# Performance work log

Measured on AMD Instinct MI355X. Metric: run time of the kernel, lower is better.

## Reference

```python
import jax, jax.numpy as jnp
import numpy as np

NUM_HEADS = 16
WINDOW = 128
PERSIST = 16


def setup_inputs() -> dict:
    key = jax.random.key(0)
    ks = jax.random.split(key, 6)
    B, S, D, L = 2, 2048, 2048, 512
    sd = 1.0 / np.sqrt(D)
    sl = 1.0 / np.sqrt(L)
    return {
        "x": jax.random.normal(ks[0], (B, S, D), dtype=jnp.float32),
        "Wq": jax.random.normal(ks[1], (D, D), dtype=jnp.float32) * sd,
        "Wkv": jax.random.normal(ks[2], (D, L), dtype=jnp.float32) * sd,
        "Wk": jax.random.normal(ks[3], (L, D), dtype=jnp.float32) * sl,
        "Wv": jax.random.normal(ks[4], (L, D), dtype=jnp.float32) * sl,
        "Wo": jax.random.normal(ks[5], (D, D), dtype=jnp.float32) * sd,
    }


def reference(x, Wq, Wkv, Wk, Wv, Wo):
    B, S, D = x.shape
    H = NUM_HEADS
    hd = D // H
    scale = hd ** -0.5

    q = (x @ Wq).reshape(B, S, H, hd)
    kv_latent = x @ Wkv                      # MLA-style latent bottleneck
    k = (kv_latent @ Wk).reshape(B, S, H, hd)
    v = (kv_latent @ Wv).reshape(B, S, H, hd)

    # causal + sliding-window + persistent attention-sink mask
    qi = jnp.arange(S)[:, None]
    ki = jnp.arange(S)[None, :]
    mask = (ki <= qi) & ((qi - ki < WINDOW) | (ki < PERSIST))  # [S,S]

    scores = jnp.einsum("bqhd,bkhd->bhqk", q, k) * scale
    scores = jnp.where(mask[None, None], scores, jnp.finfo(scores.dtype).min)
    attn = jax.nn.softmax(scores, axis=-1)
    out = jnp.einsum("bhqk,bkhd->bqhd", attn, v).reshape(B, S, D)
    return out @ Wo
```

## Files before the change

### kernel.cpp

```cpp
#include <hip/hip_runtime.h>

typedef float f32x4 __attribute__((ext_vector_type(4)));
typedef float f32x16 __attribute__((ext_vector_type(16)));
typedef __bf16 bf16x8 __attribute__((ext_vector_type(8)));

__device__ __forceinline__ short f2bf(float f) {
    union { float f; unsigned u; } x; x.f = f;
    unsigned r = x.u + 0x7fffu + ((x.u >> 16) & 1u);
    return (short)(r >> 16);
}

__device__ __forceinline__ void store_out(float* p, float v) { *p = v; }
__device__ __forceinline__ void store_out(short* p, float v) { *p = f2bf(v); }

__device__ __forceinline__ void gload_lds16(const short* g, short* l) {
    __builtin_amdgcn_global_load_lds(
        (__attribute__((address_space(1))) void*)(void*)g,
        (__attribute__((address_space(3))) void*)l, 16, 0, 0);
}

__global__ void prep_all(const float* __restrict__ x, short* __restrict__ xb,
                         const float* __restrict__ Wq, const float* __restrict__ Wkv,
                         short* __restrict__ WqkvT) {
    __shared__ float tile[32][33];
    int id = blockIdx.x;
    const int t = threadIdx.x;
    if (id < 8192) {
        const int i = id * 256 + t;
        float4 v = ((const float4*)x)[i];
        ((short4*)xb)[i] = make_short4(f2bf(v.x), f2bf(v.y), f2bf(v.z), f2bf(v.w));
        return;
    }
    id -= 8192;
    const float* in; short* out; int R, C, xt, yt;
    if (id < 4096) { in = Wq;  out = WqkvT; R = 2048; C = 2048; xt = id & 63; yt = id >> 6; }
    else           { id -= 4096; in = Wkv; out = WqkvT + (size_t)2048 * 2048;
                     R = 2048; C = 512; xt = id & 15; yt = id >> 4; }
    const int c0 = xt * 32, r0 = yt * 32;
    const int tx = t & 31, ty = t >> 5;
#pragma unroll
    for (int i = 0; i < 32; i += 8)
        tile[ty + i][tx] = in[(size_t)(r0 + ty + i) * C + c0 + tx];
    __syncthreads();
#pragma unroll
    for (int i = 0; i < 32; i += 8)
        out[(size_t)(c0 + ty + i) * R + r0 + tx] = f2bf(tile[tx][ty + i]);
}

template <typename OutT>
__device__ __forceinline__ void gemm32_core(
    const short* __restrict__ A, const short* __restrict__ Bt, OutT* __restrict__ C,
    int m0, int n0, int K, int lda, int ldb, int ldc, short* sA, short* sB) {
    const int t = threadIdx.x;
    const int w = t >> 6, l = t & 63;
    const int wr = w >> 1, wc = w & 1;
    const int lrow = l & 31, lhalf = l >> 5;

    f32x16 acc[2][2] = {};

    const int r_off = w * 32 + (l >> 3);
    const int c8 = (((l & 7) ^ (l >> 3)) & 7) * 8;
    const short* aB = A + (size_t)(m0 + r_off) * lda + c8;
    const short* bB = Bt + (size_t)(n0 + r_off) * ldb + c8;
    short* sAw = sA + w * 2048;
    short* sBw = sB + w * 2048;

    for (int kk = 0; kk < K; kk += 64) {
#pragma unroll
        for (int p = 0; p < 4; ++p) {
            gload_lds16(aB + kk + (size_t)(p * 8) * lda, sAw + p * 512);
            gload_lds16(bB + kk + (size_t)(p * 8) * ldb, sBw + p * 512);
        }
        __syncthreads();
#pragma unroll
        for (int ks = 0; ks < 4; ++ks) {
            const int c = ks * 2 + lhalf;
            bf16x8 af[2], bfr[2];
#pragma unroll
            for (int mi = 0; mi < 2; ++mi) {
                const int m = wr * 64 + mi * 32 + lrow;
                af[mi] = *(const bf16x8*)&sA[m * 64 + (c ^ (m & 7)) * 8];
            }
#pragma unroll
            for (int ni = 0; ni < 2; ++ni) {
                const int n = wc * 64 + ni * 32 + lrow;
                bfr[ni] = *(const bf16x8*)&sB[n * 64 + (c ^ (n & 7)) * 8];
            }
#pragma unroll
            for (int mi = 0; mi < 2; ++mi)
#pragma unroll
                for (int ni = 0; ni < 2; ++ni)
                    acc[mi][ni] = __builtin_amdgcn_mfma_f32_32x32x16_bf16(
                        af[mi], bfr[ni], acc[mi][ni], 0, 0, 0);
        }
        __syncthreads();
    }
#pragma unroll
    for (int mi = 0; mi < 2; ++mi)
#pragma unroll
        for (int ni = 0; ni < 2; ++ni) {
            const int col = n0 + wc * 64 + ni * 32 + lrow;
#pragma unroll
            for (int r = 0; r < 16; ++r) {
                const int row = m0 + wr * 64 + mi * 32 + (r & 3) + 8 * (r >> 2) + 4 * lhalf;
                store_out(&C[(size_t)row * ldc + col], acc[mi][ni][r]);
            }
        }
}

__global__ __launch_bounds__(256, 2)
void gemm32qkv(const short* __restrict__ A, const short* __restrict__ Bt,
               short* __restrict__ C,
               const float* __restrict__ Wo, const float* __restrict__ Wk,
               const float* __restrict__ Wv,
               short* __restrict__ WoT, short* __restrict__ WkT,
               short* __restrict__ WvT) {
    __shared__ __align__(16) short sA[128 * 64];
    __shared__ __align__(16) short sB[128 * 64];
    int id = blockIdx.x;
    if (id < 640) {
        const int sw = (id & 7) * 80 + (id >> 3);
        gemm32_core<short>(A, Bt, C, (sw / 20) * 128, (sw % 20) * 128,
                           2048, 2048, 2048, 2560, sA, sB);
        return;
    }
    id -= 640;
    float (*tile)[33] = (float(*)[33])sA;
    const float* in; short* out; int R, Cc, xt, yt;
    if (id < 4096)      { in = Wo; out = WoT; R = 2048; Cc = 2048; xt = id & 63; yt = id >> 6; }
    else if (id < 5120) { id -= 4096; in = Wk; out = WkT; R = 512; Cc = 2048; xt = id & 63; yt = id >> 6; }
    else                { id -= 5120; in = Wv; out = WvT; R = 512; Cc = 2048; xt = id & 63; yt = id >> 6; }
    const int c0 = xt * 32, r0 = yt * 32;
    const int t = threadIdx.x;
    const int tx = t & 31, ty = t >> 5;
#pragma unroll
    for (int i = 0; i < 32; i += 8)
        tile[ty + i][tx] = in[(size_t)(r0 + ty + i) * Cc + c0 + tx];
    __syncthreads();
#pragma unroll
    for (int i = 0; i < 32; i += 8)
        out[(size_t)(c0 + ty + i) * R + r0 + tx] = f2bf(tile[tx][ty + i]);
}

#define LBASE(buf, kh, ab) ((((((buf) << 1) | (kh)) << 1) | (ab)) * 8192)

#define STAGE(P, ld, tt, kh, buf, ab)                                   \
    do {                                                                \
        const int kb_ = (tt) * 64 + (kh) * 32;                          \
        const short* s_ = (P) + kb_;                                    \
        short* d_ = lds + LBASE(buf, kh, ab) + w * 512;                 \
        gload_lds16(s_, d_);                                            \
        gload_lds16(s_ + (size_t)128 * (ld), d_ + 4096);                \
    } while (0)

#define VM6 asm volatile("s_waitcnt vmcnt(6)" ::: "memory")

#define MFMA16(a, b, c) __builtin_amdgcn_mfma_f32_16x16x32_bf16(a, b, c, 0, 0, 0)

#define MM_ROW(mi, areg)                                                \
    acc[mi][0] = MFMA16(areg, bv0, acc[mi][0]);                         \
    acc[mi][1] = MFMA16(areg, bv1, acc[mi][1]);                         \
    acc[mi][2] = MFMA16(areg, bv2, acc[mi][2]);                         \
    acc[mi][3] = MFMA16(areg, bv3, acc[mi][3]);

#define HALFK(buf, kh, STG0, W0, STG1)                                  \
    {                                                                   \
        bf16x8 bv0, bv1, bv2, bv3;                                      \
        {                                                               \
            const short* Ab_ = lds + LBASE(buf, kh, 0) + (wm * 128) * 32 + foff; \
            const short* Bb_ = lds + LBASE(buf, kh, 1) + (wn * 64) * 32 + foff;  \
            bf16x8 a0_ = *(const bf16x8*)&Ab_[0];                       \
            bf16x8 a1_ = *(const bf16x8*)&Ab_[512];                     \
            bf16x8 a2_ = *(const bf16x8*)&Ab_[1024];                    \
            bf16x8 a3_ = *(const bf16x8*)&Ab_[1536];                    \
            bv0 = *(const bf16x8*)&Bb_[0];                              \
            bv1 = *(const bf16x8*)&Bb_[512];                            \
            bv2 = *(const bf16x8*)&Bb_[1024];                           \
            bv3 = *(const bf16x8*)&Bb_[1536];                           \
            STG0;                                                       \
            W0;                                                         \
            __builtin_amdgcn_s_barrier();                               \
            asm volatile("s_waitcnt lgkmcnt(0)" ::: "memory");          \
            __builtin_amdgcn_sched_barrier(0);                          \
            __builtin_amdgcn_s_setprio(1);                              \
            MM_ROW(0, a0_) MM_ROW(1, a1_) MM_ROW(2, a2_) MM_ROW(3, a3_) \
            __builtin_amdgcn_s_setprio(0);                              \
            __builtin_amdgcn_s_barrier();                               \
        }                                                               \
        {                                                               \
            const short* Ab_ = lds + LBASE(buf, kh, 0) + (wm * 128 + 64) * 32 + foff; \
            bf16x8 a0_ = *(const bf16x8*)&Ab_[0];                       \
            bf16x8 a1_ = *(const bf16x8*)&Ab_[512];                     \
            bf16x8 a2_ = *(const bf16x8*)&Ab_[1024];                    \
            bf16x8 a3_ = *(const bf16x8*)&Ab_[1536];                    \
            STG1;                                                       \
            __builtin_amdgcn_s_barrier();                               \
            asm volatile("s_waitcnt lgkmcnt(0)" ::: "memory");          \
            __builtin_amdgcn_sched_barrier(0);                          \
            __builtin_amdgcn_s_setprio(1);                              \
            MM_ROW(4, a0_) MM_ROW(5, a1_) MM_ROW(6, a2_) MM_ROW(7, a3_) \
            __builtin_amdgcn_s_setprio(0);                              \
            __builtin_amdgcn_s_barrier();                               \
        }                                                               \
    }

template <typename OutT>
__device__ __forceinline__ void gemm256_core(
    const short* __restrict__ A, const short* __restrict__ Bt, OutT* __restrict__ C,
    int m0, int n0, int K, int lda, int ldb, int ldc, short* lds) {
    const int t = threadIdx.x;
    const int w = t >> 6, l = t & 63;
    const int wm = w >> 2, wn = w & 3;
    const int l15 = l & 15, lc = l >> 4;

    const int su = (l & 7) ^ ((l >> 3) & 7);
    const int srow = (w << 4) + ((l >> 3) << 1) + (su >> 2);
    const int scol = (su & 3) << 3;
    const short* Ag = A + (size_t)(m0 + srow) * lda + scol;
    const short* Bg = Bt + (size_t)(n0 + srow) * ldb + scol;

    const int i3 = ((((l15 & 1) << 2) | lc) ^ ((l15 >> 1) & 7));
    const int foff = (l15 >> 1) * 64 + i3 * 8;

    f32x4 acc[8][4] = {};

    const int ntm1 = (K >> 6) - 1;
    const int niter = K >> 7;

    STAGE(Ag, lda, 0, 0, 0, 0);
    STAGE(Bg, ldb, 0, 0, 0, 1);
    STAGE(Ag, lda, 0, 1, 0, 0);
    STAGE(Bg, ldb, 0, 1, 0, 1);
    STAGE(Ag, lda, 1, 0, 1, 0);
    STAGE(Bg, ldb, 1, 0, 1, 1);
    asm volatile("s_waitcnt vmcnt(8)" ::: "memory");
    __builtin_amdgcn_s_barrier();

#pragma unroll 1
    for (int it = 0; it < niter; ++it) {
        const int tt = it * 2;
        const int t1 = tt + 1;
        const int t2 = (tt + 2 > ntm1) ? ntm1 : tt + 2;
        const int t3 = (tt + 3 > ntm1) ? ntm1 : tt + 3;
        HALFK(0, 0, STAGE(Ag, lda, t1, 1, 1, 0), VM6, STAGE(Bg, ldb, t1, 1, 1, 1))
        HALFK(0, 1, STAGE(Ag, lda, t2, 0, 0, 0), VM6, STAGE(Bg, ldb, t2, 0, 0, 1))
        HALFK(1, 0, STAGE(Ag, lda, t2, 1, 0, 0), VM6, STAGE(Bg, ldb, t2, 1, 0, 1))
        HALFK(1, 1, STAGE(Ag, lda, t3, 0, 1, 0), VM6, STAGE(Bg, ldb, t3, 0, 1, 1))
    }

    asm volatile("s_waitcnt vmcnt(0)" ::: "memory");

    const int crow = m0 + wm * 128 + lc * 4;
    const int ccol = n0 + wn * 64 + l15;
#pragma unroll
    for (int mi = 0; mi < 8; ++mi)
#pragma unroll
        for (int ni = 0; ni < 4; ++ni) {
            OutT* cp = C + (size_t)(crow + mi * 16) * ldc + ccol + ni * 16;
#pragma unroll
            for (int rr = 0; rr < 4; ++rr)
                store_out(cp + (size_t)rr * ldc, acc[mi][ni][rr]);
        }
}

__global__ __launch_bounds__(512, 2)
void gemm256_kv(const short* __restrict__ kvl, const short* __restrict__ WkT,
                short* __restrict__ kk, const short* __restrict__ WvT,
                short* __restrict__ vT) {
    extern __shared__ short lds[];
    int id = blockIdx.x;
    if (id < 128) {
        gemm256_core<short>(kvl, WkT, kk, (id >> 3) * 256, (id & 7) * 256,
                            512, 2560, 512, 2048, lds);
    } else {
        id -= 128;
        gemm256_core<short>(WvT, kvl, vT, (id >> 4) * 256, (id & 15) * 256,
                            512, 512, 2560, 4096, lds);
    }
}

#define LB2(s) ((s) * 12288)

#define STG2(ps, pt)                                                    \
    do {                                                                \
        const int kb_ = (pt) * 32;                                      \
        gload_lds16(Ag + kb_, lds + LB2(ps) + w * 512);                 \
        gload_lds16(Ag + kb_ + (size_t)128 * lda, lds + LB2(ps) + 4096 + w * 512); \
        gload_lds16(Bg + kb_, lds + LB2(ps) + 8192 + w * 512);          \
    } while (0)

#define PH2(s, ps, pt)                                                  \
    {                                                                   \
        const short* Ab_ = lds + LB2(s) + wm * 2048 + foff;             \
        const short* Bb_ = lds + LB2(s) + 8192 + wn * 2048 + foff;      \
        bf16x8 a0_ = *(const bf16x8*)&Ab_[0];                           \
        bf16x8 a1_ = *(const bf16x8*)&Ab_[512];                         \
        bf16x8 a2_ = *(const bf16x8*)&Ab_[1024];                        \
        bf16x8 a3_ = *(const bf16x8*)&Ab_[1536];                        \
        bf16x8 b0_ = *(const bf16x8*)&Bb_[0];                           \
        bf16x8 b1_ = *(const bf16x8*)&Bb_[512];                         \
        bf16x8 b2_ = *(const bf16x8*)&Bb_[1024];                        \
        bf16x8 b3_ = *(const bf16x8*)&Bb_[1536];                        \
        STG2(ps, pt);                                                   \
        asm volatile("s_waitcnt vmcnt(6)" ::: "memory");                \
        __builtin_amdgcn_s_barrier();                                   \
        asm volatile("s_waitcnt lgkmcnt(0)" ::: "memory");              \
        __builtin_amdgcn_sched_barrier(0);                              \
        __builtin_amdgcn_s_setprio(1);                                  \
        acc[0][0]=MFMA16(a0_,b0_,acc[0][0]); acc[0][1]=MFMA16(a0_,b1_,acc[0][1]); \
        acc[0][2]=MFMA16(a0_,b2_,acc[0][2]); acc[0][3]=MFMA16(a0_,b3_,acc[0][3]); \
        acc[1][0]=MFMA16(a1_,b0_,acc[1][0]); acc[1][1]=MFMA16(a1_,b1_,acc[1][1]); \
        acc[1][2]=MFMA16(a1_,b2_,acc[1][2]); acc[1][3]=MFMA16(a1_,b3_,acc[1][3]); \
        acc[2][0]=MFMA16(a2_,b0_,acc[2][0]); acc[2][1]=MFMA16(a2_,b1_,acc[2][1]); \
        acc[2][2]=MFMA16(a2_,b2_,acc[2][2]); acc[2][3]=MFMA16(a2_,b3_,acc[2][3]); \
        acc[3][0]=MFMA16(a3_,b0_,acc[3][0]); acc[3][1]=MFMA16(a3_,b1_,acc[3][1]); \
        acc[3][2]=MFMA16(a3_,b2_,acc[3][2]); acc[3][3]=MFMA16(a3_,b3_,acc[3][3]); \
        __builtin_amdgcn_s_setprio(0);                                  \
        __builtin_amdgcn_s_barrier();                                   \
    }

__global__ __launch_bounds__(512, 1)
void gemm_out(const short* __restrict__ A, const short* __restrict__ Bt,
              float* __restrict__ C, int K, int lda, int ldb, int ldc) {
    extern __shared__ short lds[];
    const int sw = ((int)blockIdx.x & 7) * 32 + ((int)blockIdx.x >> 3);
    const int m0 = (sw >> 4) * 256, n0 = (sw & 15) * 128;
    const int t = threadIdx.x;
    const int w = t >> 6, l = t & 63;
    const int wm = w >> 1, wn = w & 1;
    const int l15 = l & 15, lc = l >> 4;

    const int su = (l & 7) ^ ((l >> 3) & 7);
    const int srow = (w << 4) + ((l >> 3) << 1) + (su >> 2);
    const int scol = (su & 3) << 3;
    const short* Ag = A + (size_t)(m0 + srow) * lda + scol;
    const short* Bg = Bt + (size_t)(n0 + srow) * ldb + scol;

    const int i3 = ((((l15 & 1) << 2) | lc) ^ ((l15 >> 1) & 7));
    const int foff = (l15 >> 1) * 64 + i3 * 8;

    f32x4 acc[4][4] = {};

    const int nkh1 = (K >> 5) - 1;

    STG2(0, 0);
    STG2(1, 1);
    STG2(2, 2);
    asm volatile("s_waitcnt vmcnt(6)" ::: "memory");
    __builtin_amdgcn_s_barrier();

#pragma unroll 1
    for (int it = 0; it < (K >> 7); ++it) {
        const int h0 = it * 4;
        const int p3 = h0 + 3;
        const int p4 = (h0 + 4 > nkh1) ? nkh1 : h0 + 4;
        const int p5 = (h0 + 5 > nkh1) ? nkh1 : h0 + 5;
        const int p6 = (h0 + 6 > nkh1) ? nkh1 : h0 + 6;
        PH2(0, 3, p3)
        PH2(1, 0, p4)
        PH2(2, 1, p5)
        PH2(3, 2, p6)
    }

    asm volatile("s_waitcnt vmcnt(0)" ::: "memory");

    const int crow = m0 + wm * 64 + lc * 4;
    const int ccol = n0 + wn * 64 + l15;
#pragma unroll
    for (int mi = 0; mi < 4; ++mi)
#pragma unroll
        for (int ni = 0; ni < 4; ++ni) {
            float* cp = C + (size_t)(crow + mi * 16) * ldc + ccol + ni * 16;
#pragma unroll
            for (int rr = 0; rr < 4; ++rr)
                store_out(cp + (size_t)rr * ldc, acc[mi][ni][rr]);
        }
}

#define A_S 2048
#define A_D 2048
#define A_M 4096
#define A_HD 128
__global__ __launch_bounds__(256)
void attn_win3(const short* __restrict__ Q, const short* __restrict__ K,
               const short* __restrict__ vT, short* __restrict__ O, int ldq) {
    const int qt = blockIdx.x, h = blockIdx.y, b = blockIdx.z;
    const int Qs = qt * 64;
    const int t = threadIdx.x, w = t >> 6, l = t & 63;
    const int qs = Qs + w * 16;
    const int lg = l >> 4, ln = l & 15;
    const float SCALE = 0.088388347648318447f;

    __shared__ __align__(16) short sK[2][512 * 8];
    __shared__ __align__(16) short sV[2][512 * 8];
    __shared__ __align__(16) short sP[4][16][40];

    const size_t bS = (size_t)b * A_S;
    const short* qrow = Q + (bS + qs + ln) * ldq + h * A_HD;
    bf16x8 qf[4];
#pragma unroll
    for (int ks = 0; ks < 4; ++ks)
        qf[ks] = *(const bf16x8*)(qrow + ks * 32 + lg * 8);

    f32x4 o[8] = {};
    float lsum[4] = {0.f, 0.f, 0.f, 0.f};

    int C_lo = (Qs - 127) >> 5; if (C_lo < 0) C_lo = 0;
    const int C_hi = (Qs + 63) >> 5;
    const bool sink = C_lo > 0;
    const int total = (C_hi - C_lo + 1) + (sink ? 1 : 0);

    const int key0 = t >> 4, dseg0s = (t & 15) ^ (key0 & 7);
    const int d0 = t >> 2, ksg0 = (t & 3) ^ ((d0 >> 1) & 3);
    const int key1 = (256 + t) >> 4, dseg1s = (t & 15) ^ (key1 & 7);
    const int d1 = (256 + t) >> 2, ksg1 = (t & 3) ^ ((d1 >> 1) & 3);
    const short* Kb = K + bS * A_D + h * A_HD;
    const short* Vb = vT + (size_t)h * A_HD * A_M + b * A_S;

#define ASTAGE(kb, buf)                                                         \
    do {                                                                        \
        gload_lds16(Kb + (size_t)((kb) + key0) * A_D + dseg0s * 8,              \
                    &sK[buf][(size_t)(w * 64) * 8]);                            \
        gload_lds16(Vb + (size_t)d0 * A_M + (kb) + ksg0 * 8,                    \
                    &sV[buf][(size_t)(w * 64) * 8]);                            \
        gload_lds16(Kb + (size_t)((kb) + key1) * A_D + dseg1s * 8,              \
                    &sK[buf][(size_t)(256 + w * 64) * 8]);                      \
        gload_lds16(Vb + (size_t)d1 * A_M + (kb) + ksg1 * 8,                    \
                    &sV[buf][(size_t)(256 + w * 64) * 8]);                      \
    } while (0)

#define CHUNK_KB(ci) ((((sink) && (ci) == 0) ? 0 : (C_lo + (ci) - (sink ? 1 : 0))) * 32)

    ASTAGE(CHUNK_KB(0), 0);
    __syncthreads();

    for (int ci = 0; ci < total; ++ci) {
        if (ci + 1 < total) {
            const int nkb = CHUNK_KB(ci + 1);
            ASTAGE(nkb, (ci + 1) & 1);
        }
        const int kb = CHUNK_KB(ci);
        const int buf = ci & 1;
        const bool any = (kb < 16) || ((kb + 31 >= qs - 127) && (kb <= qs + 15));
        if (any) {
            f32x4 s0 = {0.f, 0.f, 0.f, 0.f}, s1 = {0.f, 0.f, 0.f, 0.f};
#pragma unroll
            for (int ks = 0; ks < 4; ++ks) {
                const int dsg = ks * 4 + lg;
                bf16x8 k0 = *(const bf16x8*)&sK[buf][(ln * 16 + (dsg ^ (ln & 7))) * 8];
                bf16x8 k1 = *(const bf16x8*)&sK[buf][((16 + ln) * 16 + (dsg ^ (ln & 7))) * 8];
                s0 = __builtin_amdgcn_mfma_f32_16x16x32_bf16(qf[ks], k0, s0, 0, 0, 0);
                s1 = __builtin_amdgcn_mfma_f32_16x16x32_bf16(qf[ks], k1, s1, 0, 0, 0);
            }
            const int k0i = kb + ln, k1i = kb + 16 + ln;
#pragma unroll
            for (int r = 0; r < 4; ++r) {
                const int qi = qs + lg * 4 + r;
                const bool m0 = (k0i <= qi) && ((qi - k0i < 128) || (k0i < 16));
                const bool m1 = (k1i <= qi) && ((qi - k1i < 128) || (k1i < 16));
                const float p0 = m0 ? __expf(s0[r] * SCALE) : 0.f;
                const float p1 = m1 ? __expf(s1[r] * SCALE) : 0.f;
                lsum[r] += p0 + p1;
                sP[w][lg * 4 + r][ln] = f2bf(p0);
                sP[w][lg * 4 + r][16 + ln] = f2bf(p1);
            }
            bf16x8 pf = *(const bf16x8*)&sP[w][ln][lg * 8];
#pragma unroll
            for (int dgi = 0; dgi < 8; ++dgi) {
                const int d = dgi * 16 + ln;
                bf16x8 vf = *(const bf16x8*)&sV[buf][(d * 4 + (lg ^ ((ln >> 1) & 3))) * 8];
                o[dgi] = __builtin_amdgcn_mfma_f32_16x16x32_bf16(pf, vf, o[dgi], 0, 0, 0);
            }
        }
        __syncthreads();
    }
#undef ASTAGE
#undef CHUNK_KB

#pragma unroll
    for (int r = 0; r < 4; ++r) {
        float s = lsum[r];
        s += __shfl_xor(s, 1); s += __shfl_xor(s, 2);
        s += __shfl_xor(s, 4); s += __shfl_xor(s, 8);
        const float inv = 1.0f / s;
        short* orow = O + (bS + qs + lg * 4 + r) * A_D + h * A_HD + ln;
#pragma unroll
        for (int dgi = 0; dgi < 8; ++dgi)
            orow[dgi * 16] = f2bf(o[dgi][r] * inv);
    }
}

extern "C" void kernel_launch(void* const* d_in, const int* in_sizes, int n_in,
                              void* d_out, int out_size, void* d_ws, size_t ws_size,
                              hipStream_t stream) {
    (void)in_sizes; (void)n_in; (void)out_size; (void)ws_size;
    const float* x   = (const float*)d_in[0];
    const float* Wq  = (const float*)d_in[1];
    const float* Wkv = (const float*)d_in[2];
    const float* Wk  = (const float*)d_in[3];
    const float* Wv  = (const float*)d_in[4];
    const float* Wo  = (const float*)d_in[5];
    float* out = (float*)d_out;

    const int B = 2, S = 2048, D = 2048, L = 512, H = 16;
    const int M = B * S;
    const int NQ = D + L;

    short* p = (short*)d_ws;
    short* xb    = p; p += (size_t)M * D;
    short* WqkvT = p; p += (size_t)NQ * D;
    short* WkT   = p; p += (size_t)D * L;
    short* WvT   = p; p += (size_t)D * L;
    short* WoT   = p; p += (size_t)D * D;
    short* qkv   = p; p += (size_t)M * NQ;
    short* kk    = p; p += (size_t)M * D;
    short* vT    = p; p += (size_t)D * M;
    short* ao    = p; p += (size_t)M * D;

    static bool attr_done = false;
    if (!attr_done) {
        hipFuncSetAttribute((const void*)&gemm256_kv,
                            hipFuncAttributeMaxDynamicSharedMemorySize, 131072);
        hipFuncSetAttribute((const void*)&gemm_out,
                            hipFuncAttributeMaxDynamicSharedMemorySize, 98304);
        attr_done = true;
    }

    prep_all<<<13312, 256, 0, stream>>>(x, xb, Wq, Wkv, WqkvT);
    gemm32qkv<<<6784, 256, 0, stream>>>(xb, WqkvT, qkv, Wo, Wk, Wv,
                                        WoT, WkT, WvT);
    gemm256_kv<<<256, 512, 131072, stream>>>(qkv + D, WkT, kk, WvT, vT);

    attn_win3<<<dim3(S / 64, H, B), 256, 0, stream>>>(qkv, kk, vT, ao, NQ);

    gemm_out<<<256, 512, 98304, stream>>>(ao, WoT, out, D, D, D, D);
}
```

Measured before the change: 264.1 us.

## Replace 128x128 QKV GEMM with pipelined 256x160 tiled kernel, move weight prep

The fused QKV projection GEMM moves from a 128x128 tile kernel using 32x32 MFMA with a simple load-sync loop to a 256x160 tile kernel with 512 threads. The new kernel uses a four-stage LDS pipeline, 16x16x32 MFMA and barrier/priority scheduling, and its 256 blocks map exactly onto the 4096x2560 output. The Wo/Wk/Wv transposes move out of the GEMM launch and into prep_all. The goal is better data reuse and load/compute overlap than the old grid. The risks are one-block-per-CU occupancy and the odd 4-byte loads needed for the extra 32 B rows.

Result: faster. 253.5 us (-4.0%).

```diff
diff --git a/kernel.cpp b/kernel.cpp
--- a/kernel.cpp
+++ b/kernel.cpp
@@ -1,7 +1,6 @@
 #include <hip/hip_runtime.h>
 
 typedef float f32x4 __attribute__((ext_vector_type(4)));
-typedef float f32x16 __attribute__((ext_vector_type(16)));
 typedef __bf16 bf16x8 __attribute__((ext_vector_type(8)));
 
 __device__ __forceinline__ short f2bf(float f) {
@@ -18,10 +17,18 @@
         (__attribute__((address_space(1))) void*)(void*)g,
         (__attribute__((address_space(3))) void*)l, 16, 0, 0);
 }
+__device__ __forceinline__ void gload_lds4(const short* g, short* l) {
+    __builtin_amdgcn_global_load_lds(
+        (__attribute__((address_space(1))) void*)(void*)g,
+        (__attribute__((address_space(3))) void*)l, 4, 0, 0);
+}
 
 __global__ void prep_all(const float* __restrict__ x, short* __restrict__ xb,
-                         const float* __restrict__ Wq, const float* __restrict__ Wkv,
-                         short* __restrict__ WqkvT) {
+                         const float* __restrict__ Wq, const float* __restrict__ Wo,
+                         const float* __restrict__ Wk, const float* __restrict__ Wv,
+                         const float* __restrict__ Wkv,
+                         short* __restrict__ WqkvT, short* __restrict__ WoT,
+                         short* __restrict__ WkT, short* __restrict__ WvT) {
     __shared__ float tile[32][33];
     int id = blockIdx.x;
     const int t = threadIdx.x;
@@ -33,9 +40,12 @@
     }
     id -= 8192;
     const float* in; short* out; int R, C, xt, yt;
-    if (id < 4096) { in = Wq;  out = WqkvT; R = 2048; C = 2048; xt = id & 63; yt = id >> 6; }
-    else           { id -= 4096; in = Wkv; out = WqkvT + (size_t)2048 * 2048;
-                     R = 2048; C = 512; xt = id & 15; yt = id >> 4; }
+    if (id < 4096)       { in = Wq;  out = WqkvT; R = 2048; C = 2048; xt = id & 63; yt = id >> 6; }
+    else if (id < 8192)  { id -= 4096; in = Wo;  out = WoT;  R = 2048; C = 2048; xt = id & 63; yt = id >> 6; }
+    else if (id < 9216)  { id -= 8192; in = Wk;  out = WkT;  R = 512;  C = 2048; xt = id & 63; yt = id >> 6; }
+    else if (id < 10240) { id -= 9216; in = Wv;  out = WvT;  R = 512;  C = 2048; xt = id & 63; yt = id >> 6; }
+    else                 { id -= 10240; in = Wkv; out = WqkvT + (size_t)2048 * 2048;
+                           R = 2048; C = 512; xt = id & 15; yt = id >> 4; }
     const int c0 = xt * 32, r0 = yt * 32;
     const int tx = t & 31, ty = t >> 5;
 #pragma unroll
@@ -47,100 +57,7 @@
         out[(size_t)(c0 + ty + i) * R + r0 + tx] = f2bf(tile[tx][ty + i]);
 }
 
-template <typename OutT>
-__device__ __forceinline__ void gemm32_core(
-    const short* __restrict__ A, const short* __restrict__ Bt, OutT* __restrict__ C,
-    int m0, int n0, int K, int lda, int ldb, int ldc, short* sA, short* sB) {
-    const int t = threadIdx.x;
-    const int w = t >> 6, l = t & 63;
-    const int wr = w >> 1, wc = w & 1;
-    const int lrow = l & 31, lhalf = l >> 5;
-
-    f32x16 acc[2][2] = {};
-
-    const int r_off = w * 32 + (l >> 3);
-    const int c8 = (((l & 7) ^ (l >> 3)) & 7) * 8;
-    const short* aB = A + (size_t)(m0 + r_off) * lda + c8;
-    const short* bB = Bt + (size_t)(n0 + r_off) * ldb + c8;
-    short* sAw = sA + w * 2048;
-    short* sBw = sB + w * 2048;
-
-    for (int kk = 0; kk < K; kk += 64) {
-#pragma unroll
-        for (int p = 0; p < 4; ++p) {
-            gload_lds16(aB + kk + (size_t)(p * 8) * lda, sAw + p * 512);
-            gload_lds16(bB + kk + (size_t)(p * 8) * ldb, sBw + p * 512);
-        }
-        __syncthreads();
-#pragma unroll
-        for (int ks = 0; ks < 4; ++ks) {
-            const int c = ks * 2 + lhalf;
-            bf16x8 af[2], bfr[2];
-#pragma unroll
-            for (int mi = 0; mi < 2; ++mi) {
-                const int m = wr * 64 + mi * 32 + lrow;
-                af[mi] = *(const bf16x8*)&sA[m * 64 + (c ^ (m & 7)) * 8];
-            }
-#pragma unroll
-            for (int ni = 0; ni < 2; ++ni) {
-                const int n = wc * 64 + ni * 32 + lrow;
-                bfr[ni] = *(const bf16x8*)&sB[n * 64 + (c ^ (n & 7)) * 8];
-            }
-#pragma unroll
-            for (int mi = 0; mi < 2; ++mi)
-#pragma unroll
-                for (int ni = 0; ni < 2; ++ni)
-                    acc[mi][ni] = __builtin_amdgcn_mfma_f32_32x32x16_bf16(
-                        af[mi], bfr[ni], acc[mi][ni], 0, 0, 0);
-        }
-        __syncthreads();
-    }
-#pragma unroll
-    for (int mi = 0; mi < 2; ++mi)
-#pragma unroll
-        for (int ni = 0; ni < 2; ++ni) {
-            const int col = n0 + wc * 64 + ni * 32 + lrow;
-#pragma unroll
-            for (int r = 0; r < 16; ++r) {
-                const int row = m0 + wr * 64 + mi * 32 + (r & 3) + 8 * (r >> 2) + 4 * lhalf;
-                store_out(&C[(size_t)row * ldc + col], acc[mi][ni][r]);
-            }
-        }
-}
-
-__global__ __launch_bounds__(256, 2)
-void gemm32qkv(const short* __restrict__ A, const short* __restrict__ Bt,
-               short* __restrict__ C,
-               const float* __restrict__ Wo, const float* __restrict__ Wk,
-               const float* __restrict__ Wv,
-               short* __restrict__ WoT, short* __restrict__ WkT,
-               short* __restrict__ WvT) {
-    __shared__ __align__(16) short sA[128 * 64];
-    __shared__ __align__(16) short sB[128 * 64];
-    int id = blockIdx.x;
-    if (id < 640) {
-        const int sw = (id & 7) * 80 + (id >> 3);
-        gemm32_core<short>(A, Bt, C, (sw / 20) * 128, (sw % 20) * 128,
-                           2048, 2048, 2048, 2560, sA, sB);
-        return;
-    }
-    id -= 640;
-    float (*tile)[33] = (float(*)[33])sA;
-    const float* in; short* out; int R, Cc, xt, yt;
-    if (id < 4096)      { in = Wo; out = WoT; R = 2048; Cc = 2048; xt = id & 63; yt = id >> 6; }
-    else if (id < 5120) { id -= 4096; in = Wk; out = WkT; R = 512; Cc = 2048; xt = id & 63; yt = id >> 6; }
-    else                { id -= 5120; in = Wv; out = WvT; R = 512; Cc = 2048; xt = id & 63; yt = id >> 6; }
-    const int c0 = xt * 32, r0 = yt * 32;
-    const int t = threadIdx.x;
-    const int tx = t & 31, ty = t >> 5;
-#pragma unroll
-    for (int i = 0; i < 32; i += 8)
-        tile[ty + i][tx] = in[(size_t)(r0 + ty + i) * Cc + c0 + tx];
-    __syncthreads();
-#pragma unroll
-    for (int i = 0; i < 32; i += 8)
-        out[(size_t)(c0 + ty + i) * R + r0 + tx] = f2bf(tile[tx][ty + i]);
-}
+#define MFMA16(a, b, c) __builtin_amdgcn_mfma_f32_16x16x32_bf16(a, b, c, 0, 0, 0)
 
 #define LBASE(buf, kh, ab) ((((((buf) << 1) | (kh)) << 1) | (ab)) * 8192)
 
@@ -154,8 +71,6 @@
     } while (0)
 
 #define VM6 asm volatile("s_waitcnt vmcnt(6)" ::: "memory")
-
-#define MFMA16(a, b, c) __builtin_amdgcn_mfma_f32_16x16x32_bf16(a, b, c, 0, 0, 0)
 
 #define MM_ROW(mi, areg)                                                \
     acc[mi][0] = MFMA16(areg, bv0, acc[mi][0]);                         \
@@ -279,6 +194,110 @@
     }
 }
 
+#define LQ(s) ((s) * 13312)
+
+#define QSTG(ps, pt)                                                    \
+    do {                                                                \
+        const int kb_ = (pt) * 32;                                      \
+        gload_lds16(Ag + kb_, lds + LQ(ps) + w * 512);                  \
+        gload_lds16(Ag + kb_ + (size_t)128 * lda, lds + LQ(ps) + 4096 + w * 512); \
+        gload_lds16(Bg + kb_, lds + LQ(ps) + 8192 + w * 512);           \
+        gload_lds4(B4 + kb_, lds + LQ(ps) + 12288 + w * 128);           \
+    } while (0)
+
+#define QPH(s, ps, pt)                                                  \
+    {                                                                   \
+        const short* Ab_ = lds + LQ(s) + wm * 2048 + foff;              \
+        const short* Bb_ = lds + LQ(s) + 8192 + wn * 2560 + foff;       \
+        bf16x8 a0_ = *(const bf16x8*)&Ab_[0];                           \
+        bf16x8 a1_ = *(const bf16x8*)&Ab_[512];                         \
+        bf16x8 a2_ = *(const bf16x8*)&Ab_[1024];                        \
+        bf16x8 a3_ = *(const bf16x8*)&Ab_[1536];                        \
+        bf16x8 b0_ = *(const bf16x8*)&Bb_[0];                           \
+        bf16x8 b1_ = *(const bf16x8*)&Bb_[512];                         \
+        bf16x8 b2_ = *(const bf16x8*)&Bb_[1024];                        \
+        bf16x8 b3_ = *(const bf16x8*)&Bb_[1536];                        \
+        bf16x8 b4_ = *(const bf16x8*)&Bb_[2048];                        \
+        QSTG(ps, pt);                                                   \
+        asm volatile("s_waitcnt vmcnt(8)" ::: "memory");                \
+        __builtin_amdgcn_s_barrier();                                   \
+        asm volatile("s_waitcnt lgkmcnt(0)" ::: "memory");              \
+        __builtin_amdgcn_sched_barrier(0);                              \
+        __builtin_amdgcn_s_setprio(1);                                  \
+        acc[0][0]=MFMA16(a0_,b0_,acc[0][0]); acc[0][1]=MFMA16(a0_,b1_,acc[0][1]); \
+        acc[0][2]=MFMA16(a0_,b2_,acc[0][2]); acc[0][3]=MFMA16(a0_,b3_,acc[0][3]); \
+        acc[0][4]=MFMA16(a0_,b4_,acc[0][4]);                            \
+        acc[1][0]=MFMA16(a1_,b0_,acc[1][0]); acc[1][1]=MFMA16(a1_,b1_,acc[1][1]); \
+        acc[1][2]=MFMA16(a1_,b2_,acc[1][2]); acc[1][3]=MFMA16(a1_,b3_,acc[1][3]); \
+        acc[1][4]=MFMA16(a1_,b4_,acc[1][4]);                            \
+        acc[2][0]=MFMA16(a2_,b0_,acc[2][0]); acc[2][1]=MFMA16(a2_,b1_,acc[2][1]); \
+        acc[2][2]=MFMA16(a2_,b2_,acc[2][2]); acc[2][3]=MFMA16(a2_,b3_,acc[2][3]); \
+        acc[2][4]=MFMA16(a2_,b4_,acc[2][4]);                            \
+        acc[3][0]=MFMA16(a3_,b0_,acc[3][0]); acc[3][1]=MFMA16(a3_,b1_,acc[3][1]); \
+        acc[3][2]=MFMA16(a3_,b2_,acc[3][2]); acc[3][3]=MFMA16(a3_,b3_,acc[3][3]); \
+        acc[3][4]=MFMA16(a3_,b4_,acc[3][4]);                            \
+        __builtin_amdgcn_s_setprio(0);                                  \
+        __builtin_amdgcn_s_barrier();                                   \
+    }
+
+__global__ __launch_bounds__(512, 1)
+void gemm_qkv160(const short* __restrict__ A, const short* __restrict__ Bt,
+                 short* __restrict__ C, int K, int lda, int ldb, int ldc) {
+    extern __shared__ short lds[];
+    const int sw = ((int)blockIdx.x & 7) * 32 + ((int)blockIdx.x >> 3);
+    const int m0 = (sw >> 4) * 256, n0 = (sw & 15) * 160;
+    const int t = threadIdx.x;
+    const int w = t >> 6, l = t & 63;
+    const int wm = w >> 1, wn = w & 1;
+    const int l15 = l & 15, lc = l >> 4;
+
+    const int su = (l & 7) ^ ((l >> 3) & 7);
+    const int srow = (w << 4) + ((l >> 3) << 1) + (su >> 2);
+    const int scol = (su & 3) << 3;
+    const short* Ag = A + (size_t)(m0 + srow) * lda + scol;
+    const short* Bg = Bt + (size_t)(n0 + srow) * ldb + scol;
+    const int u4 = ((t >> 2) & 7) ^ ((t >> 5) & 7);
+    const int b4row = 128 + ((t >> 5) << 1) + (u4 >> 2);
+    const int b4off = ((u4 & 3) << 3) + ((t & 3) << 1);
+    const short* B4 = Bt + (size_t)(n0 + b4row) * ldb + b4off;
+
+    const int i3 = ((((l15 & 1) << 2) | lc) ^ ((l15 >> 1) & 7));
+    const int foff = (l15 >> 1) * 64 + i3 * 8;
+
+    f32x4 acc[4][5] = {};
+    const int last = (K >> 5) - 1;
+
+    QSTG(0, 0); QSTG(1, 1); QSTG(2, 2);
+    asm volatile("s_waitcnt vmcnt(8)" ::: "memory");
+    __builtin_amdgcn_s_barrier();
+
+#pragma unroll 1
+    for (int it = 0; it < (K >> 7); ++it) {
+        const int h0 = it * 4;
+        const int q3 = h0 + 3;
+        const int q4 = (h0 + 4 > last) ? last : h0 + 4;
+        const int q5 = (h0 + 5 > last) ? last : h0 + 5;
+        const int q6 = (h0 + 6 > last) ? last : h0 + 6;
+        QPH(0, 3, q3)
+        QPH(1, 0, q4)
+        QPH(2, 1, q5)
+        QPH(3, 2, q6)
+    }
+    asm volatile("s_waitcnt vmcnt(0)" ::: "memory");
+
+    const int crow = m0 + wm * 64 + lc * 4;
+    const int ccol = n0 + wn * 80 + l15;
+#pragma unroll
+    for (int mi = 0; mi < 4; ++mi)
+#pragma unroll
+        for (int ni = 0; ni < 5; ++ni) {
+            short* cp = C + (size_t)(crow + mi * 16) * ldc + ccol + ni * 16;
+#pragma unroll
+            for (int rr = 0; rr < 4; ++rr)
+                store_out(cp + (size_t)rr * ldc, acc[mi][ni][rr]);
+        }
+}
+
 #define LB2(s) ((s) * 12288)
 
 #define STG2(ps, pt)                                                    \
@@ -521,14 +540,16 @@
     if (!attr_done) {
         hipFuncSetAttribute((const void*)&gemm256_kv,
                             hipFuncAttributeMaxDynamicSharedMemorySize, 131072);
+        hipFuncSetAttribute((const void*)&gemm_qkv160,
+                            hipFuncAttributeMaxDynamicSharedMemorySize, 106496);
         hipFuncSetAttribute((const void*)&gemm_out,
                             hipFuncAttributeMaxDynamicSharedMemorySize, 98304);
         attr_done = true;
     }
 
-    prep_all<<<13312, 256, 0, stream>>>(x, xb, Wq, Wkv, WqkvT);
-    gemm32qkv<<<6784, 256, 0, stream>>>(xb, WqkvT, qkv, Wo, Wk, Wv,
-                                        WoT, WkT, WvT);
+    prep_all<<<19456, 256, 0, stream>>>(x, xb, Wq, Wo, Wk, Wv, Wkv,
+                                        WqkvT, WoT, WkT, WvT);
+    gemm_qkv160<<<256, 512, 106496, stream>>>(xb, WqkvT, qkv, D, D, D, NQ);
     gemm256_kv<<<256, 512, 131072, stream>>>(qkv + D, WkT, kk, WvT, vT);
 
     attn_win3<<<dim3(S / 64, H, B), 256, 0, stream>>>(qkv, kk, vT, ao, NQ);
```
